# Optimization experiments

Hardware: AMD Instinct MI355X
Metric: run time of the kernel (lower is better)

The kernel has to match this reference:

```python
import jax, jax.numpy as jnp
import numpy as np

B, N, S, C1, C2 = 8, 8192, 2048, 128, 256
H1, H2 = 256, 256
EPS_LN = 1e-5


def _layernorm_c(x, g, b):
    # LayerNorm over channel dim of [B, C, N]
    mu = jnp.mean(x, axis=1, keepdims=True)
    var = jnp.mean((x - mu) ** 2, axis=1, keepdims=True)
    return g[None, :, None] * (x - mu) / jnp.sqrt(var + EPS_LN) + b[None, :, None]


def setup_inputs() -> dict:
    key = jax.random.key(0)
    ks = jax.random.split(key, 8)
    Cin = C1 + C2
    return {
        "points_coor1": jax.random.normal(ks[0], (B, 3, N), jnp.float32),
        "points_coor2": jax.random.normal(ks[1], (B, 3, S), jnp.float32),
        "points_fea1": jax.random.normal(ks[2], (B, C1, N), jnp.float32),
        "points_fea2": jax.random.normal(ks[3], (B, C2, S), jnp.float32),
        "points_padding2": jnp.zeros((B, S), dtype=bool),
        "W1": jax.random.normal(ks[4], (H1, Cin), jnp.float32) * 0.05,
        "b1": jnp.zeros((H1,), jnp.float32),
        "g1": jnp.ones((H1,), jnp.float32),
        "be1": jnp.zeros((H1,), jnp.float32),
        "W2": jax.random.normal(ks[5], (H2, H1), jnp.float32) * 0.05,
        "b2": jnp.zeros((H2,), jnp.float32),
        "g2": jnp.ones((H2,), jnp.float32),
        "be2": jnp.zeros((H2,), jnp.float32),
    }


def reference(points_coor1, points_coor2, points_fea1, points_fea2,
              points_padding2, W1, b1, g1, be1, W2, b2, g2, be2):
    c1 = jnp.transpose(points_coor1, (0, 2, 1))  # [B,N,3]
    c2 = jnp.transpose(points_coor2, (0, 2, 1))  # [B,S,3]
    f2 = jnp.transpose(points_fea2, (0, 2, 1))   # [B,S,C2]

    # push padded points far away (max computed on unmodified coords, as in torch RHS-first eval)
    big = jnp.max(jnp.abs(c2)) * 3.0
    c2 = jnp.where(points_padding2[..., None], big, c2)

    # squared euclidean pairwise distances [B,N,S]
    d = (jnp.sum(c1 * c1, -1)[:, :, None]
         + jnp.sum(c2 * c2, -1)[:, None, :]
         - 2.0 * jnp.einsum('bnd,bsd->bns', c1, c2))

    neg_d, idx = jax.lax.top_k(-d, 3)          # 3 smallest distances
    dists = -neg_d                              # [B,N,3]
    recip = 1.0 / jnp.clip(dists, 1e-8)
    w = recip / jnp.sum(recip, axis=-1, keepdims=True)  # [B,N,3]

    gathered = jax.vmap(lambda f, i: f[i])(f2, idx)     # [B,N,3,C2]
    interp = jnp.einsum('bnkc,bnk->bcn', gathered, w)   # [B,C2,N]

    x = jnp.concatenate([points_fea1, interp], axis=1)  # [B,C1+C2,N]
    x = jax.nn.relu(_layernorm_c(jnp.einsum('oc,bcn->bon', W1, x) + b1[None, :, None], g1, be1))
    x = jax.nn.relu(_layernorm_c(jnp.einsum('oc,bcn->bon', W2, x) + b2[None, :, None], g2, be2))
    return x
```

## Files before the change

### kernel.cpp

```cpp
#include <hip/hip_runtime.h>
#include <stdint.h>

#define BB 8
#define NPT 8192
#define SPT 2048
#define C1D 128
#define C2D 256
#define CIN 384
#define HD 256
#define SPLIT 8
#define SC (SPT/SPLIT)

typedef __attribute__((ext_vector_type(8))) short bf16x8;
typedef __attribute__((ext_vector_type(4))) float f32x4;

__device__ __forceinline__ unsigned short f2b(float f){
  unsigned int u = __float_as_uint(f);
  u += 0x7fffu + ((u >> 16) & 1u);
  return (unsigned short)(u >> 16);
}

__global__ __launch_bounds__(256) void cvt2_bf16_kernel(const float* __restrict__ W1,
    const float* __restrict__ W2, unsigned short* __restrict__ dst){
  int i = blockIdx.x * 256 + threadIdx.x;
  const int n1 = HD * CIN;
  if (i < n1) dst[i] = f2b(W1[i]);
  else {
    int k = i - n1;
    if (k < HD * HD) dst[n1 + k] = f2b(W2[k]);
  }
}

__global__ __launch_bounds__(256) void gsrc_kernel(const float* __restrict__ coor2,
    const unsigned char* __restrict__ pad, float4* __restrict__ gs){
  int i = blockIdx.x * 256 + threadIdx.x;
  int b = i >> 11, s = i & (SPT - 1);
  const float* cb = coor2 + b * 3 * SPT;
  float x = cb[s], y = cb[SPT + s], z = cb[2*SPT + s];
  if (pad[i]) { x = 1e19f; y = 1e19f; z = 1e19f; }
  float n2 = __fadd_rn(__fadd_rn(__fmul_rn(x,x), __fmul_rn(y,y)), __fmul_rn(z,z));
  gs[i] = make_float4(x, y, z, n2);
}

__global__ __launch_bounds__(256) void transpose_cn(const float* __restrict__ src,
    unsigned short* __restrict__ dst, int Cdim, int Ndim, int dstStride){
  __shared__ unsigned short t[32][33];
  int b = blockIdx.z;
  int n0 = blockIdx.x * 32, c0 = blockIdx.y * 32;
  int tx = threadIdx.x, ty = threadIdx.y;
  const float* s = src + (size_t)b * Cdim * Ndim;
  unsigned short* d = dst + (size_t)b * Ndim * dstStride;
  #pragma unroll
  for (int i = 0; i < 4; i++)
    t[ty + i*8][tx] = f2b(s[(size_t)(c0 + ty + i*8) * Ndim + n0 + tx]);
  __syncthreads();
  #pragma unroll
  for (int i = 0; i < 4; i++)
    d[(size_t)(n0 + ty + i*8) * dstStride + c0 + tx] = t[tx][ty + i*8];
}

__global__ __launch_bounds__(256) void knn_part_kernel(const float* __restrict__ coor1,
    const float4* __restrict__ gs, float* __restrict__ cv, int* __restrict__ cj){
  int b = blockIdx.y, c = blockIdx.z;
  int s0c = c * SC;
  const float4* gsb = gs + b * SPT + s0c;
  int n = blockIdx.x * 256 + threadIdx.x;
  const float* ca = coor1 + b * 3 * NPT;
  float x1 = ca[n], y1 = ca[NPT + n], z1 = ca[2*NPT + n];
  float n1 = __fadd_rn(__fadd_rn(__fmul_rn(x1,x1), __fmul_rn(y1,y1)), __fmul_rn(z1,z1));
  float v0 = 3.4e38f, v1 = 3.4e38f, v2 = 3.4e38f;
  int j0 = 0, j1 = 0, j2 = 0;
  #pragma unroll 8
  for (int s = 0; s < SC; s++){
    float4 q = gsb[s];
    float dot = __fadd_rn(__fadd_rn(__fmul_rn(x1,q.x), __fmul_rn(y1,q.y)), __fmul_rn(z1,q.z));
    float npn = __fadd_rn(n1, q.w);
    float d = __builtin_fmaf(-2.0f, dot, npn);
    bool l0 = d < v0, l1 = d < v1, l2 = d < v2;
    j2 = l1 ? j1 : (l2 ? s : j2);
    j1 = l0 ? j0 : (l1 ? s : j1);
    j0 = l0 ? s  : j0;
    float nv2 = __builtin_amdgcn_fmed3f(v1, v2, d);
    float nv1 = __builtin_amdgcn_fmed3f(v0, v1, d);
    v0 = fminf(v0, d); v1 = nv1; v2 = nv2;
  }
  size_t m = (size_t)b * NPT + n;
  size_t base = (m * SPLIT + c) * 3;
  cv[base+0] = v0; cv[base+1] = v1; cv[base+2] = v2;
  cj[base+0] = s0c + j0; cj[base+1] = s0c + j1; cj[base+2] = s0c + j2;
}

__global__ __launch_bounds__(256) void knn_merge_kernel(const float* __restrict__ cv,
    const int* __restrict__ cj, float* __restrict__ w3, int* __restrict__ i3){
  size_t m = (size_t)blockIdx.x * 256 + threadIdx.x;
  float v0 = 3.4e38f, v1 = 3.4e38f, v2 = 3.4e38f;
  int j0 = 0, j1 = 0, j2 = 0;
  #pragma unroll
  for (int c = 0; c < SPLIT; c++){
    #pragma unroll
    for (int k = 0; k < 3; k++){
      float d = cv[(m * SPLIT + c) * 3 + k];
      int j   = cj[(m * SPLIT + c) * 3 + k];
      bool l0 = d < v0, l1 = d < v1, l2 = d < v2;
      j2 = l1 ? j1 : (l2 ? j : j2);
      j1 = l0 ? j0 : (l1 ? j : j1);
      j0 = l0 ? j  : j0;
      float nv2 = __builtin_amdgcn_fmed3f(v1, v2, d);
      float nv1 = __builtin_amdgcn_fmed3f(v0, v1, d);
      v0 = fminf(v0, d); v1 = nv1; v2 = nv2;
    }
  }
  float r0 = 1.0f / fmaxf(v0, 1e-8f);
  float r1 = 1.0f / fmaxf(v1, 1e-8f);
  float r2 = 1.0f / fmaxf(v2, 1e-8f);
  float rs = (r0 + r1) + r2;
  w3[m*3+0] = r0 / rs; w3[m*3+1] = r1 / rs; w3[m*3+2] = r2 / rs;
  i3[m*3+0] = j0; i3[m*3+1] = j1; i3[m*3+2] = j2;
}

__global__ __launch_bounds__(256) void interp_kernel(const unsigned short* __restrict__ f2t,
    const float* __restrict__ w3, const int* __restrict__ i3, unsigned short* __restrict__ xpm){
  int m = blockIdx.x * 4 + (threadIdx.x >> 6);
  int lane = threadIdx.x & 63;
  int b = m >> 13;
  int s0 = i3[m*3+0], s1 = i3[m*3+1], s2 = i3[m*3+2];
  float w0 = w3[m*3+0], w1 = w3[m*3+1], w2 = w3[m*3+2];
  const ushort4 a = *(const ushort4*)(f2t + (size_t)(b*SPT + s0) * C2D + lane*4);
  const ushort4 c = *(const ushort4*)(f2t + (size_t)(b*SPT + s1) * C2D + lane*4);
  const ushort4 e = *(const ushort4*)(f2t + (size_t)(b*SPT + s2) * C2D + lane*4);
  #define B2F(u) __uint_as_float(((unsigned int)(u)) << 16)
  ushort4 o;
  o.x = f2b(w0*B2F(a.x) + w1*B2F(c.x) + w2*B2F(e.x));
  o.y = f2b(w0*B2F(a.y) + w1*B2F(c.y) + w2*B2F(e.y));
  o.z = f2b(w0*B2F(a.z) + w1*B2F(c.z) + w2*B2F(e.z));
  o.w = f2b(w0*B2F(a.w) + w1*B2F(c.w) + w2*B2F(e.w));
  *(ushort4*)(xpm + (size_t)m * CIN + C1D + lane*4) = o;
}

__global__ __launch_bounds__(256) void mlp1_kernel(const unsigned short* __restrict__ xpm,
    const unsigned short* __restrict__ Wg, const float* __restrict__ bg,
    const float* __restrict__ gg, const float* __restrict__ beg,
    unsigned short* __restrict__ Hg){
  __shared__ __align__(16) unsigned short Ws[256*40];
  __shared__ __align__(16) unsigned short Xs[64*40];
  __shared__ float sB[256], sG[256], sBe[256];
  int tid = threadIdx.x;
  int m0 = blockIdx.x * 64;
  sB[tid] = bg[tid]; sG[tid] = gg[tid]; sBe[tid] = beg[tid];
  int w = tid >> 6, lane = tid & 63, col = lane & 15, quad = lane >> 4;
  f32x4 acc[16];
  #pragma unroll
  for (int i = 0; i < 16; i++) acc[i] = (f32x4)0.0f;
  for (int kb = 0; kb < CIN; kb += 32){
    __syncthreads();
    {
      const int4* s4 = (const int4*)(Wg + (size_t)tid * CIN + kb);
      int4* d4 = (int4*)(Ws + tid * 40);
      #pragma unroll
      for (int i = 0; i < 4; i++) d4[i] = s4[i];
    }
    {
      int mr = tid >> 2, part = tid & 3;
      *(int4*)(Xs + mr*40 + part*8) = *(const int4*)(xpm + (size_t)(m0 + mr) * CIN + kb + part*8);
    }
    __syncthreads();
    bf16x8 bfrag = *(const bf16x8*)(Xs + (w*16 + col)*40 + quad*8);
    #pragma unroll
    for (int ot = 0; ot < 16; ot++){
      bf16x8 afrag = *(const bf16x8*)(Ws + (ot*16 + col)*40 + quad*8);
      acc[ot] = __builtin_amdgcn_mfma_f32_16x16x32_bf16(afrag, bfrag, acc[ot], 0, 0, 0);
    }
  }
  float s1 = 0.f, s2 = 0.f;
  #pragma unroll
  for (int ot = 0; ot < 16; ot++)
    #pragma unroll
    for (int r = 0; r < 4; r++){
      int o = ot*16 + quad*4 + r;
      float v = acc[ot][r] + sB[o];
      acc[ot][r] = v;
      s1 += v; s2 += v*v;
    }
  s1 += __shfl_xor(s1, 16); s1 += __shfl_xor(s1, 32);
  s2 += __shfl_xor(s2, 16); s2 += __shfl_xor(s2, 32);
  float mu = s1 * (1.f/256.f);
  float rinv = rsqrtf(s2 * (1.f/256.f) - mu*mu + 1e-5f);
  unsigned short* Hb = Ws;
  for (int half = 0; half < 2; half++){
    __syncthreads();
    #pragma unroll
    for (int ot8 = 0; ot8 < 8; ot8++){
      int ot = half*8 + ot8;
      int ob = ot*16 + quad*4;
      ushort4 hv;
      hv.x = f2b(fmaxf((acc[ot][0] - mu) * rinv * sG[ob+0] + sBe[ob+0], 0.f));
      hv.y = f2b(fmaxf((acc[ot][1] - mu) * rinv * sG[ob+1] + sBe[ob+1], 0.f));
      hv.z = f2b(fmaxf((acc[ot][2] - mu) * rinv * sG[ob+2] + sBe[ob+2], 0.f));
      hv.w = f2b(fmaxf((acc[ot][3] - mu) * rinv * sG[ob+3] + sBe[ob+3], 0.f));
      *(ushort4*)(Hb + (w*16 + col)*136 + ot8*16 + quad*4) = hv;
    }
    __syncthreads();
    int mr = tid >> 2, part = tid & 3;
    #pragma unroll
    for (int r = 0; r < 4; r++){
      int piece = part*4 + r;
      *(int4*)(Hg + (size_t)(m0 + mr)*HD + half*128 + piece*8) = *(const int4*)(Hb + mr*136 + piece*8);
    }
  }
}

__global__ __launch_bounds__(256) void mlp2_kernel(const unsigned short* __restrict__ Hg,
    const unsigned short* __restrict__ Wg, const float* __restrict__ bg,
    const float* __restrict__ gg, const float* __restrict__ beg,
    float* __restrict__ outg){
  __shared__ __align__(16) unsigned short Ws[256*40];
  __shared__ __align__(16) unsigned short Xs[64*40];
  __shared__ float sB[256], sG[256], sBe[256];
  int tid = threadIdx.x;
  int m0 = blockIdx.x * 64;
  int b = m0 >> 13, n0 = m0 & (NPT - 1);
  sB[tid] = bg[tid]; sG[tid] = gg[tid]; sBe[tid] = beg[tid];
  int w = tid >> 6, lane = tid & 63, col = lane & 15, quad = lane >> 4;
  f32x4 acc[16];
  #pragma unroll
  for (int i = 0; i < 16; i++) acc[i] = (f32x4)0.0f;
  for (int kb = 0; kb < HD; kb += 32){
    __syncthreads();
    {
      const int4* s4 = (const int4*)(Wg + (size_t)tid * HD + kb);
      int4* d4 = (int4*)(Ws + tid * 40);
      #pragma unroll
      for (int i = 0; i < 4; i++) d4[i] = s4[i];
    }
    {
      int mr = tid >> 2, part = tid & 3;
      *(int4*)(Xs + mr*40 + part*8) = *(const int4*)(Hg + (size_t)(m0 + mr) * HD + kb + part*8);
    }
    __syncthreads();
    bf16x8 bfrag = *(const bf16x8*)(Xs + (w*16 + col)*40 + quad*8);
    #pragma unroll
    for (int ot = 0; ot < 16; ot++){
      bf16x8 afrag = *(const bf16x8*)(Ws + (ot*16 + col)*40 + quad*8);
      acc[ot] = __builtin_amdgcn_mfma_f32_16x16x32_bf16(afrag, bfrag, acc[ot], 0, 0, 0);
    }
  }
  float s1 = 0.f, s2 = 0.f;
  #pragma unroll
  for (int ot = 0; ot < 16; ot++)
    #pragma unroll
    for (int r = 0; r < 4; r++){
      int o = ot*16 + quad*4 + r;
      float v = acc[ot][r] + sB[o];
      acc[ot][r] = v;
      s1 += v; s2 += v*v;
    }
  s1 += __shfl_xor(s1, 16); s1 += __shfl_xor(s1, 32);
  s2 += __shfl_xor(s2, 16); s2 += __shfl_xor(s2, 32);
  float mu = s1 * (1.f/256.f);
  float rinv = rsqrtf(s2 * (1.f/256.f) - mu*mu + 1e-5f);
  size_t obase = (size_t)b * HD * NPT + n0 + w*16 + col;
  #pragma unroll
  for (int ot = 0; ot < 16; ot++)
    #pragma unroll
    for (int r = 0; r < 4; r++){
      int o = ot*16 + quad*4 + r;
      float v = (acc[ot][r] - mu) * rinv * sG[o] + sBe[o];
      outg[obase + (size_t)o * NPT] = fmaxf(v, 0.f);
    }
}

extern "C" void kernel_launch(void* const* d_in, const int* in_sizes, int n_in,
                              void* d_out, int out_size, void* d_ws, size_t ws_size,
                              hipStream_t stream){
  const float* coor1 = (const float*)d_in[0];
  const float* coor2 = (const float*)d_in[1];
  const float* fea1  = (const float*)d_in[2];
  const float* fea2  = (const float*)d_in[3];
  const unsigned char* pad = (const unsigned char*)d_in[4];
  const float* W1  = (const float*)d_in[5];
  const float* b1  = (const float*)d_in[6];
  const float* g1  = (const float*)d_in[7];
  const float* be1 = (const float*)d_in[8];
  const float* W2  = (const float*)d_in[9];
  const float* b2  = (const float*)d_in[10];
  const float* g2  = (const float*)d_in[11];
  const float* be2 = (const float*)d_in[12];
  float* out = (float*)d_out;

  char* ws = (char*)d_ws;
  float* w3            = (float*)(ws + 256);
  int*   i3            = (int*)  (ws + 786688);
  unsigned short* W1b  = (unsigned short*)(ws + 1573120);
  unsigned short* W2b  = (unsigned short*)(ws + 1769728);
  unsigned short* f2t  = (unsigned short*)(ws + 1900800);
  unsigned short* xpm  = (unsigned short*)(ws + 10289408);
  unsigned short* Hg   = (unsigned short*)(ws + 60621056);
  float* cv            = (float*)(ws + 60621056);
  int*   cj            = (int*)  (ws + 60621056 + 6291456);
  float4* gs           = (float4*)(ws + 60621056 + 16777216);

  cvt2_bf16_kernel<<<(HD*CIN + HD*HD + 255)/256, 256, 0, stream>>>(W1, W2, W1b);
  gsrc_kernel<<<BB*SPT/256, 256, 0, stream>>>(coor2, pad, gs);
  dim3 tb(32, 8);
  transpose_cn<<<dim3(SPT/32, C2D/32, BB), tb, 0, stream>>>(fea2, f2t, C2D, SPT, C2D);
  transpose_cn<<<dim3(NPT/32, C1D/32, BB), tb, 0, stream>>>(fea1, xpm, C1D, NPT, CIN);
  knn_part_kernel<<<dim3(NPT/256, BB, SPLIT), 256, 0, stream>>>(coor1, gs, cv, cj);
  knn_merge_kernel<<<BB*NPT/256, 256, 0, stream>>>(cv, cj, w3, i3);
  interp_kernel<<<BB*NPT/4, 256, 0, stream>>>(f2t, w3, i3, xpm);
  mlp1_kernel<<<BB*NPT/64, 256, 0, stream>>>(xpm, W1b, b1, g1, be1, Hg);
  mlp2_kernel<<<BB*NPT/64, 256, 0, stream>>>(Hg, W2b, b2, g2, be2, out);
}
```

Baseline: 287.4 us.

## Fuse the two MLP layers into one kernel keeping hidden activations in LDS

Merges mlp1 and mlp2 into one kernel. The 64-row hidden activation tile stays in shared memory (Hbuf, padded stride 264) and feeds the second GEMM directly, so the bf16 hidden tensor is never written to or read back from global memory. This also removes one kernel launch. In exchange LDS use per block grows to about 33KB plus the weight tile, which may lower occupancy, and the second layer's weight tile is still reloaded for every K step.

```diff
diff --git a/kernel.cpp b/kernel.cpp
--- a/kernel.cpp
+++ b/kernel.cpp
@@ -137,24 +137,29 @@
   *(ushort4*)(xpm + (size_t)m * CIN + C1D + lane*4) = o;
 }
 
-__global__ __launch_bounds__(256) void mlp1_kernel(const unsigned short* __restrict__ xpm,
-    const unsigned short* __restrict__ Wg, const float* __restrict__ bg,
-    const float* __restrict__ gg, const float* __restrict__ beg,
-    unsigned short* __restrict__ Hg){
+__global__ __launch_bounds__(256) void mlp_fused_kernel(const unsigned short* __restrict__ xpm,
+    const unsigned short* __restrict__ W1g, const unsigned short* __restrict__ W2g,
+    const float* __restrict__ b1, const float* __restrict__ g1, const float* __restrict__ be1,
+    const float* __restrict__ b2, const float* __restrict__ g2, const float* __restrict__ be2,
+    float* __restrict__ outg){
   __shared__ __align__(16) unsigned short Ws[256*40];
-  __shared__ __align__(16) unsigned short Xs[64*40];
+  __shared__ __align__(16) unsigned short Hbuf[64*264];
   __shared__ float sB[256], sG[256], sBe[256];
+  unsigned short* Xs = Hbuf;
   int tid = threadIdx.x;
   int m0 = blockIdx.x * 64;
-  sB[tid] = bg[tid]; sG[tid] = gg[tid]; sBe[tid] = beg[tid];
+  int b = m0 >> 13, n0 = m0 & (NPT - 1);
+  sB[tid] = b1[tid]; sG[tid] = g1[tid]; sBe[tid] = be1[tid];
   int w = tid >> 6, lane = tid & 63, col = lane & 15, quad = lane >> 4;
+  int ml = w*16 + col;
   f32x4 acc[16];
   #pragma unroll
   for (int i = 0; i < 16; i++) acc[i] = (f32x4)0.0f;
+
   for (int kb = 0; kb < CIN; kb += 32){
     __syncthreads();
     {
-      const int4* s4 = (const int4*)(Wg + (size_t)tid * CIN + kb);
+      const int4* s4 = (const int4*)(W1g + (size_t)tid * CIN + kb);
       int4* d4 = (int4*)(Ws + tid * 40);
       #pragma unroll
       for (int i = 0; i < 4; i++) d4[i] = s4[i];
@@ -164,80 +169,55 @@
       *(int4*)(Xs + mr*40 + part*8) = *(const int4*)(xpm + (size_t)(m0 + mr) * CIN + kb + part*8);
     }
     __syncthreads();
-    bf16x8 bfrag = *(const bf16x8*)(Xs + (w*16 + col)*40 + quad*8);
+    bf16x8 bfrag = *(const bf16x8*)(Xs + ml*40 + quad*8);
     #pragma unroll
     for (int ot = 0; ot < 16; ot++){
       bf16x8 afrag = *(const bf16x8*)(Ws + (ot*16 + col)*40 + quad*8);
       acc[ot] = __builtin_amdgcn_mfma_f32_16x16x32_bf16(afrag, bfrag, acc[ot], 0, 0, 0);
     }
   }
-  float s1 = 0.f, s2 = 0.f;
-  #pragma unroll
-  for (int ot = 0; ot < 16; ot++)
-    #pragma unroll
-    for (int r = 0; r < 4; r++){
-      int o = ot*16 + quad*4 + r;
-      float v = acc[ot][r] + sB[o];
-      acc[ot][r] = v;
-      s1 += v; s2 += v*v;
-    }
-  s1 += __shfl_xor(s1, 16); s1 += __shfl_xor(s1, 32);
-  s2 += __shfl_xor(s2, 16); s2 += __shfl_xor(s2, 32);
-  float mu = s1 * (1.f/256.f);
-  float rinv = rsqrtf(s2 * (1.f/256.f) - mu*mu + 1e-5f);
-  unsigned short* Hb = Ws;
-  for (int half = 0; half < 2; half++){
-    __syncthreads();
-    #pragma unroll
-    for (int ot8 = 0; ot8 < 8; ot8++){
-      int ot = half*8 + ot8;
+  {
+    float s1 = 0.f, s2 = 0.f;
+    #pragma unroll
+    for (int ot = 0; ot < 16; ot++)
+      #pragma unroll
+      for (int r = 0; r < 4; r++){
+        int o = ot*16 + quad*4 + r;
+        float v = acc[ot][r] + sB[o];
+        acc[ot][r] = v;
+        s1 += v; s2 += v*v;
+      }
+    s1 += __shfl_xor(s1, 16); s1 += __shfl_xor(s1, 32);
+    s2 += __shfl_xor(s2, 16); s2 += __shfl_xor(s2, 32);
+    float mu = s1 * (1.f/256.f);
+    float rinv = rsqrtf(s2 * (1.f/256.f) - mu*mu + 1e-5f);
+    __syncthreads();
+    #pragma unroll
+    for (int ot = 0; ot < 16; ot++){
       int ob = ot*16 + quad*4;
       ushort4 hv;
       hv.x = f2b(fmaxf((acc[ot][0] - mu) * rinv * sG[ob+0] + sBe[ob+0], 0.f));
       hv.y = f2b(fmaxf((acc[ot][1] - mu) * rinv * sG[ob+1] + sBe[ob+1], 0.f));
       hv.z = f2b(fmaxf((acc[ot][2] - mu) * rinv * sG[ob+2] + sBe[ob+2], 0.f));
       hv.w = f2b(fmaxf((acc[ot][3] - mu) * rinv * sG[ob+3] + sBe[ob+3], 0.f));
-      *(ushort4*)(Hb + (w*16 + col)*136 + ot8*16 + quad*4) = hv;
-    }
-    __syncthreads();
-    int mr = tid >> 2, part = tid & 3;
-    #pragma unroll
-    for (int r = 0; r < 4; r++){
-      int piece = part*4 + r;
-      *(int4*)(Hg + (size_t)(m0 + mr)*HD + half*128 + piece*8) = *(const int4*)(Hb + mr*136 + piece*8);
-    }
-  }
-}
-
-__global__ __launch_bounds__(256) void mlp2_kernel(const unsigned short* __restrict__ Hg,
-    const unsigned short* __restrict__ Wg, const float* __restrict__ bg,
-    const float* __restrict__ gg, const float* __restrict__ beg,
-    float* __restrict__ outg){
-  __shared__ __align__(16) unsigned short Ws[256*40];
-  __shared__ __align__(16) unsigned short Xs[64*40];
-  __shared__ float sB[256], sG[256], sBe[256];
-  int tid = threadIdx.x;
-  int m0 = blockIdx.x * 64;
-  int b = m0 >> 13, n0 = m0 & (NPT - 1);
-  sB[tid] = bg[tid]; sG[tid] = gg[tid]; sBe[tid] = beg[tid];
-  int w = tid >> 6, lane = tid & 63, col = lane & 15, quad = lane >> 4;
-  f32x4 acc[16];
+      *(ushort4*)(Hbuf + ml*264 + ot*16 + quad*4) = hv;
+    }
+  }
+  __syncthreads();
+  sB[tid] = b2[tid]; sG[tid] = g2[tid]; sBe[tid] = be2[tid];
+
   #pragma unroll
   for (int i = 0; i < 16; i++) acc[i] = (f32x4)0.0f;
   for (int kb = 0; kb < HD; kb += 32){
     __syncthreads();
     {
-      const int4* s4 = (const int4*)(Wg + (size_t)tid * HD + kb);
+      const int4* s4 = (const int4*)(W2g + (size_t)tid * HD + kb);
       int4* d4 = (int4*)(Ws + tid * 40);
       #pragma unroll
       for (int i = 0; i < 4; i++) d4[i] = s4[i];
     }
-    {
-      int mr = tid >> 2, part = tid & 3;
-      *(int4*)(Xs + mr*40 + part*8) = *(const int4*)(Hg + (size_t)(m0 + mr) * HD + kb + part*8);
-    }
-    __syncthreads();
-    bf16x8 bfrag = *(const bf16x8*)(Xs + (w*16 + col)*40 + quad*8);
+    __syncthreads();
+    bf16x8 bfrag = *(const bf16x8*)(Hbuf + ml*264 + kb + quad*8);
     #pragma unroll
     for (int ot = 0; ot < 16; ot++){
       bf16x8 afrag = *(const bf16x8*)(Ws + (ot*16 + col)*40 + quad*8);
@@ -294,7 +274,6 @@
   unsigned short* W2b  = (unsigned short*)(ws + 1769728);
   unsigned short* f2t  = (unsigned short*)(ws + 1900800);
   unsigned short* xpm  = (unsigned short*)(ws + 10289408);
-  unsigned short* Hg   = (unsigned short*)(ws + 60621056);
   float* cv            = (float*)(ws + 60621056);
   int*   cj            = (int*)  (ws + 60621056 + 6291456);
   float4* gs           = (float4*)(ws + 60621056 + 16777216);
@@ -307,6 +286,5 @@
   knn_part_kernel<<<dim3(NPT/256, BB, SPLIT), 256, 0, stream>>>(coor1, gs, cv, cj);
   knn_merge_kernel<<<BB*NPT/256, 256, 0, stream>>>(cv, cj, w3, i3);
   interp_kernel<<<BB*NPT/4, 256, 0, stream>>>(f2t, w3, i3, xpm);
-  mlp1_kernel<<<BB*NPT/64, 256, 0, stream>>>(xpm, W1b, b1, g1, be1, Hg);
-  mlp2_kernel<<<BB*NPT/64, 256, 0, stream>>>(Hg, W2b, b2, g2, be2, out);
-}
+  mlp_fused_kernel<<<BB*NPT/64, 256, 0, stream>>>(xpm, W1b, W2b, b1, g1, be1, b2, g2, be2, out);
+}
```

After: 262.3 us. 1.1x faster.
